# Kernel tuning notes

Measured on AMD Instinct MI355X. Metric: run time of the kernel, lower is better.

The kernel has to match this reference:

```python
import jax, jax.numpy as jnp
import numpy as np

B, T, C = 8, 2048, 1024
NEG_INF = -1e38


def setup_inputs() -> dict:
    key = jax.random.key(0)
    ks = jax.random.split(key, 10)
    s = 1.0 / np.sqrt(C)
    return {
        "x": jax.random.normal(ks[0], (B, T, C), jnp.float32),
        "Wk": jax.random.normal(ks[1], (C, C), jnp.float32) * s,
        "Wv": jax.random.normal(ks[2], (C, C), jnp.float32) * s,
        "Wr": jax.random.normal(ks[3], (C, C), jnp.float32) * s,
        "Wo": jax.random.normal(ks[4], (C, C), jnp.float32) * s,
        "time_decay": jax.random.normal(ks[5], (C,), jnp.float32) * 0.5,
        "time_first": jax.random.normal(ks[6], (C,), jnp.float32) * 0.5,
        "time_mix_key": jax.random.uniform(ks[7], (1, 1, C), jnp.float32),
        "time_mix_value": jax.random.uniform(ks[8], (1, 1, C), jnp.float32),
        "time_mix_receptance": jax.random.uniform(ks[9], (1, 1, C), jnp.float32),
    }


def _wkv(k, v, time_decay, time_first):
    # k, v: [B, T, C]; numerically-stabilized exp-sum recurrence over T
    w = -jnp.exp(time_decay)  # [C]
    u = time_first            # [C]

    def step(carry, kv):
        num, den, mx = carry
        kt, vt = kv  # [B, C]
        # output at this step uses u bonus
        m_out = jnp.maximum(mx, kt + u)
        e1 = jnp.exp(mx - m_out)
        e2 = jnp.exp(kt + u - m_out)
        out = (e1 * num + e2 * vt) / (e1 * den + e2)
        # state update with decay w
        m_new = jnp.maximum(mx + w, kt)
        e1 = jnp.exp(mx + w - m_new)
        e2 = jnp.exp(kt - m_new)
        return (e1 * num + e2 * vt, e1 * den + e2, m_new), out

    init = (jnp.zeros((B, C), jnp.float32),
            jnp.zeros((B, C), jnp.float32),
            jnp.full((B, C), NEG_INF, jnp.float32))
    kT = jnp.swapaxes(k, 0, 1)  # [T, B, C]
    vT = jnp.swapaxes(v, 0, 1)
    _, outs = jax.lax.scan(step, init, (kT, vT))
    return jnp.swapaxes(outs, 0, 1)  # [B, T, C]


def reference(x, Wk, Wv, Wr, Wo, time_decay, time_first,
              time_mix_key, time_mix_value, time_mix_receptance):
    # time_shift: prev_x[t] = x[t-1], zero at t=0
    prev_x = jnp.concatenate([jnp.zeros_like(x[:, :1]), x[:, :-1]], axis=1)

    r_in = x * time_mix_receptance + prev_x * (1 - time_mix_receptance)
    k_in = x * time_mix_key + prev_x * (1 - time_mix_key)
    v_in = x * time_mix_value + prev_x * (1 - time_mix_value)

    receptance = jnp.einsum('btc,dc->btd', r_in, Wr)
    key = jnp.einsum('btc,dc->btd', k_in, Wk)
    value = jnp.einsum('btc,dc->btd', v_in, Wv)

    wkv = _wkv(key, value, time_decay, time_first)
    rwkv = jax.nn.sigmoid(receptance) * wkv
    return jnp.einsum('btc,dc->btd', rwkv, Wo)
```

## Files before the change

### kernel.cpp

```cpp
#include <hip/hip_runtime.h>
#include <cstdint>
#include <cstddef>

#define DEVI __device__ __forceinline__

typedef __attribute__((ext_vector_type(8))) short short8;
typedef __attribute__((ext_vector_type(4))) float f32x4;

constexpr int Bc = 8, Tc = 2048, Cc = 1024;
constexpr int WKV_L = 32, WKV_NCH = 64;

DEVI unsigned short f2b(float f) {
  unsigned int u = __float_as_uint(f);
  unsigned int r = (u + 0x7FFFu + ((u >> 16) & 1u)) >> 16;
  return (unsigned short)r;
}
DEVI float b2f(unsigned short u) {
  return __uint_as_float(((unsigned int)u) << 16);
}

DEVI void gload16(const unsigned short* g, unsigned short* l) {
  __builtin_amdgcn_global_load_lds(
      (const __attribute__((address_space(1))) void*)g,
      (__attribute__((address_space(3))) void*)l, 16, 0, 0);
}

__global__ void convert_bf16_kernel(const float* __restrict__ in,
                                    unsigned short* __restrict__ out, int n4) {
  int i = blockIdx.x * blockDim.x + threadIdx.x;
  if (i >= n4) return;
  const float4 v = ((const float4*)in)[i];
  ushort4 o;
  o.x = f2b(v.x); o.y = f2b(v.y); o.z = f2b(v.z); o.w = f2b(v.w);
  ((ushort4*)out)[i] = o;
}

__global__ void mix3_kernel(const float* __restrict__ x,
                            const float* __restrict__ tmk,
                            const float* __restrict__ tmv,
                            const float* __restrict__ tmr,
                            unsigned short* __restrict__ kin,
                            unsigned short* __restrict__ vin,
                            unsigned short* __restrict__ rin,
                            long n4) {
  long i = (long)blockIdx.x * blockDim.x + threadIdx.x;
  const long stride = (long)gridDim.x * blockDim.x;
  for (; i < n4; i += stride) {
    const long e = i * 4;
    const int c = (int)(e & (Cc - 1));
    const long bt = e >> 10;
    const int t = (int)(bt & (Tc - 1));
    const float4 xv = *(const float4*)(x + e);
    float4 pv = {0.f, 0.f, 0.f, 0.f};
    if (t > 0) pv = *(const float4*)(x + e - Cc);
    const float4 mk = *(const float4*)(tmk + c);
    const float4 mv = *(const float4*)(tmv + c);
    const float4 mr = *(const float4*)(tmr + c);
    const float* xp = (const float*)&xv;
    const float* pp = (const float*)&pv;
    const float* mkp = (const float*)&mk;
    const float* mvp = (const float*)&mv;
    const float* mrp = (const float*)&mr;
    ushort4 ko, vo, ro;
    unsigned short* kop = (unsigned short*)&ko;
    unsigned short* vop = (unsigned short*)&vo;
    unsigned short* rop = (unsigned short*)&ro;
#pragma unroll
    for (int q = 0; q < 4; ++q) {
      kop[q] = f2b(xp[q] * mkp[q] + pp[q] * (1.f - mkp[q]));
      vop[q] = f2b(xp[q] * mvp[q] + pp[q] * (1.f - mvp[q]));
      rop[q] = f2b(xp[q] * mrp[q] + pp[q] * (1.f - mrp[q]));
    }
    *(ushort4*)(kin + e) = ko;
    *(ushort4*)(vin + e) = vo;
    *(ushort4*)(rin + e) = ro;
  }
}

template <typename OutT>
__global__ __launch_bounds__(512, 2)
void gemm256(const unsigned short* __restrict__ A0,
             const unsigned short* __restrict__ W0, OutT* __restrict__ C0,
             const unsigned short* __restrict__ A1,
             const unsigned short* __restrict__ W1, OutT* __restrict__ C1,
             const unsigned short* __restrict__ A2,
             const unsigned short* __restrict__ W2, OutT* __restrict__ C2,
             int K, int N) {
  constexpr int BK = 64;
  __shared__ alignas(16) unsigned short As[2][256 * BK];
  __shared__ alignas(16) unsigned short Bs[2][256 * BK];
  const int z = blockIdx.z;
  const unsigned short* A = z == 0 ? A0 : (z == 1 ? A1 : A2);
  const unsigned short* W = z == 0 ? W0 : (z == 1 ? W1 : W2);
  OutT* C_out = z == 0 ? C0 : (z == 1 ? C1 : C2);
  const int m0 = blockIdx.x * 256;
  const int n0 = blockIdx.y * 256;
  const int tid = threadIdx.x;
  const int lane = tid & 63;
  const int w = tid >> 6;
  const int wm = w >> 2;
  const int wn = w & 3;
  const int fr = lane & 15;
  const int ksl = lane >> 4;

  f32x4 acc[8][4];
#pragma unroll
  for (int i = 0; i < 8; ++i)
#pragma unroll
    for (int j = 0; j < 4; ++j) acc[i][j] = (f32x4){0.f, 0.f, 0.f, 0.f};

#define STAGE(buf, kt)                                                        \
  {                                                                           \
    _Pragma("unroll")                                                         \
    for (int cc = 0; cc < 4; ++cc) {                                          \
      const int c = w * 256 + cc * 64 + lane;                                 \
      const int row = c >> 3;                                                 \
      const int gsl = (c & 7) ^ (row & 7);                                    \
      gload16(A + (size_t)(m0 + row) * K + (kt) + gsl * 8,                    \
              &As[buf][(w * 256 + cc * 64) * 8]);                             \
      gload16(W + (size_t)(n0 + row) * K + (kt) + gsl * 8,                    \
              &Bs[buf][(w * 256 + cc * 64) * 8]);                             \
    }                                                                         \
  }

  const int nt = K / BK;
  STAGE(0, 0);
  int cur = 0;
  for (int t = 0; t < nt; ++t) {
    asm volatile("s_waitcnt vmcnt(0)" ::: "memory");
    __builtin_amdgcn_s_barrier();
    asm volatile("" ::: "memory");
    if (t + 1 < nt) STAGE(cur ^ 1, (t + 1) * BK);
#pragma unroll
    for (int ks = 0; ks < 2; ++ks) {
      const int sl = ks * 4 + ksl;
      short8 af[8], bf[4];
#pragma unroll
      for (int i = 0; i < 8; ++i) {
        const int row = wm * 128 + i * 16 + fr;
        af[i] = *(const short8*)&As[cur][row * 64 + ((sl ^ (row & 7)) * 8)];
      }
#pragma unroll
      for (int j = 0; j < 4; ++j) {
        const int row = wn * 64 + j * 16 + fr;
        bf[j] = *(const short8*)&Bs[cur][row * 64 + ((sl ^ (row & 7)) * 8)];
      }
      __builtin_amdgcn_s_setprio(1);
#pragma unroll
      for (int i = 0; i < 8; ++i)
#pragma unroll
        for (int j = 0; j < 4; ++j)
          acc[i][j] = __builtin_amdgcn_mfma_f32_16x16x32_bf16(af[i], bf[j],
                                                              acc[i][j], 0, 0, 0);
      __builtin_amdgcn_s_setprio(0);
    }
    asm volatile("" ::: "memory");
    cur ^= 1;
  }
#undef STAGE

  const int orow = (lane >> 4) * 4;
  const int ocol = lane & 15;
#pragma unroll
  for (int i = 0; i < 8; ++i)
#pragma unroll
    for (int j = 0; j < 4; ++j) {
      const size_t rbase = (size_t)(m0 + wm * 128 + i * 16 + orow);
      const int cb = n0 + wn * 64 + j * 16 + ocol;
#pragma unroll
      for (int q = 0; q < 4; ++q) {
        const float vq = acc[i][j][q];
        if constexpr (sizeof(OutT) == 2)
          C_out[(rbase + q) * N + cb] = (OutT)f2b(vq);
        else
          C_out[(rbase + q) * N + cb] = (OutT)vq;
      }
    }
}

__global__ void wkv_phase1(const unsigned short* __restrict__ keyb,
                           const unsigned short* __restrict__ valb,
                           const float* __restrict__ td,
                           float* __restrict__ s_num,
                           float* __restrict__ s_den,
                           float* __restrict__ s_mx) {
  const int g = blockIdx.x * blockDim.x + threadIdx.x;
  const int c = g & (Cc - 1);
  const int j = (g / Cc) & (WKV_NCH - 1);
  const int b = g / (Cc * WKV_NCH);
  const float w = -__expf(td[c]);
  float num = 0.f, den = 0.f, mx = -1e38f;
  size_t idx = ((size_t)b * Tc + (size_t)j * WKV_L) * Cc + c;
#pragma unroll 4
  for (int i = 0; i < WKV_L; ++i, idx += Cc) {
    const float kt = b2f(keyb[idx]);
    const float vt = b2f(valb[idx]);
    const float mw = mx + w;
    const float mn = fmaxf(mw, kt);
    const float a1 = __expf(mw - mn);
    const float a2 = __expf(kt - mn);
    num = a1 * num + a2 * vt;
    den = a1 * den + a2;
    mx = mn;
  }
  s_num[g] = num; s_den[g] = den; s_mx[g] = mx;
}

__global__ void wkv_phase2(const float* __restrict__ td,
                           float* __restrict__ s_num,
                           float* __restrict__ s_den,
                           float* __restrict__ s_mx) {
  const int g = blockIdx.x * blockDim.x + threadIdx.x;
  const int c = g & (Cc - 1);
  const int b = g / Cc;
  const float Lw = -__expf(td[c]) * (float)WKV_L;
  float num = 0.f, den = 0.f, mx = -1e38f;
  size_t base = (size_t)b * WKV_NCH * Cc + c;
  for (int j = 0; j < WKV_NCH; ++j) {
    const size_t s = base + (size_t)j * Cc;
    const float ln = s_num[s], ld = s_den[s], lm = s_mx[s];
    s_num[s] = num; s_den[s] = den; s_mx[s] = mx;
    const float md = mx + Lw;
    const float m = fmaxf(md, lm);
    const float e1 = __expf(md - m);
    const float e2 = __expf(lm - m);
    num = e1 * num + e2 * ln;
    den = e1 * den + e2 * ld;
    mx = m;
  }
}

__global__ void wkv_phase3(const unsigned short* __restrict__ keyb,
                           const unsigned short* __restrict__ valb,
                           const unsigned short* __restrict__ recb,
                           const float* __restrict__ td,
                           const float* __restrict__ tf,
                           const float* __restrict__ s_num,
                           const float* __restrict__ s_den,
                           const float* __restrict__ s_mx,
                           unsigned short* __restrict__ rwkv) {
  const int g = blockIdx.x * blockDim.x + threadIdx.x;
  const int c = g & (Cc - 1);
  const int j = (g / Cc) & (WKV_NCH - 1);
  const int b = g / (Cc * WKV_NCH);
  const float w = -__expf(td[c]);
  const float u = tf[c];
  float num = s_num[g], den = s_den[g], mx = s_mx[g];
  size_t idx = ((size_t)b * Tc + (size_t)j * WKV_L) * Cc + c;
#pragma unroll 2
  for (int i = 0; i < WKV_L; ++i, idx += Cc) {
    const float kt = b2f(keyb[idx]);
    const float vt = b2f(valb[idx]);
    const float rt = b2f(recb[idx]);
    const float ku = kt + u;
    const float mo = fmaxf(mx, ku);
    const float e1 = __expf(mx - mo);
    const float e2 = __expf(ku - mo);
    const float out = (e1 * num + e2 * vt) / (e1 * den + e2);
    const float sr = 1.f / (1.f + __expf(-rt));
    rwkv[idx] = f2b(sr * out);
    const float mw = mx + w;
    const float mn = fmaxf(mw, kt);
    const float a1 = __expf(mw - mn);
    const float a2 = __expf(kt - mn);
    num = a1 * num + a2 * vt;
    den = a1 * den + a2;
    mx = mn;
  }
}

extern "C" void kernel_launch(void* const* d_in, const int* in_sizes, int n_in,
                              void* d_out, int out_size, void* d_ws, size_t ws_size,
                              hipStream_t stream) {
  const float* x   = (const float*)d_in[0];
  const float* Wk  = (const float*)d_in[1];
  const float* Wv  = (const float*)d_in[2];
  const float* Wr  = (const float*)d_in[3];
  const float* Wo  = (const float*)d_in[4];
  const float* td  = (const float*)d_in[5];
  const float* tf  = (const float*)d_in[6];
  const float* tmk = (const float*)d_in[7];
  const float* tmv = (const float*)d_in[8];
  const float* tmr = (const float*)d_in[9];

  const long BT = (long)Bc * Tc;
  const long NE = BT * Cc;
  const long CC = (long)Cc * Cc;

  char* p = (char*)d_ws;
  unsigned short* Wk_b = (unsigned short*)p; p += CC * 2;
  unsigned short* Wv_b = (unsigned short*)p; p += CC * 2;
  unsigned short* Wr_b = (unsigned short*)p; p += CC * 2;
  unsigned short* Wo_b = (unsigned short*)p; p += CC * 2;
  unsigned short* kin  = (unsigned short*)p; p += NE * 2;
  unsigned short* vin  = (unsigned short*)p; p += NE * 2;
  unsigned short* rin  = (unsigned short*)p; p += NE * 2;
  unsigned short* keyb = (unsigned short*)p; p += NE * 2;
  unsigned short* valb = (unsigned short*)p; p += NE * 2;
  unsigned short* recb = (unsigned short*)p; p += NE * 2;
  unsigned short* rwkv = kin;
  const long NS = (long)Bc * WKV_NCH * Cc;
  float* s_num = (float*)vin;
  float* s_den = s_num + NS;
  float* s_mx  = s_den + NS;

  {
    const int n4 = (int)(CC / 4);
    dim3 g((n4 + 255) / 256), b_(256);
    convert_bf16_kernel<<<g, b_, 0, stream>>>(Wk, Wk_b, n4);
    convert_bf16_kernel<<<g, b_, 0, stream>>>(Wv, Wv_b, n4);
    convert_bf16_kernel<<<g, b_, 0, stream>>>(Wr, Wr_b, n4);
    convert_bf16_kernel<<<g, b_, 0, stream>>>(Wo, Wo_b, n4);
  }

  mix3_kernel<<<2048, 256, 0, stream>>>(x, tmk, tmv, tmr, kin, vin, rin, NE / 4);

  {
    dim3 grid((unsigned)(BT / 256), (unsigned)(Cc / 256), 3), blk(512);
    gemm256<unsigned short><<<grid, blk, 0, stream>>>(
        kin, Wk_b, keyb, vin, Wv_b, valb, rin, Wr_b, recb, Cc, Cc);
  }

  wkv_phase1<<<2048, 256, 0, stream>>>(keyb, valb, td, s_num, s_den, s_mx);
  wkv_phase2<<<32, 256, 0, stream>>>(td, s_num, s_den, s_mx);
  wkv_phase3<<<2048, 256, 0, stream>>>(keyb, valb, recb, td, tf,
                                       s_num, s_den, s_mx, rwkv);

  {
    dim3 grid((unsigned)(BT / 256), (unsigned)(Cc / 256), 1), blk(512);
    gemm256<float><<<grid, blk, 0, stream>>>(
        rwkv, Wo_b, (float*)d_out, rwkv, Wo_b, (float*)d_out,
        rwkv, Wo_b, (float*)d_out, Cc, Cc);
  }
}
```

Baseline: 266.9 us.

## Interleave LDS fragment loads with MFMAs, merge weight converts, single-exp WKV updates

The GEMM inner loop is restructured so LDS reads for the next group of fragments are issued between MFMA groups, with the k-slice split into halves. The intent is to hide LDS latency behind matrix math. It also drops the s_setprio calls. The four weight-conversion launches are merged into one 2D-grid launch to cut launch overhead. The WKV recurrences now compute a single exp per max-stabilised step by branching on which operand is larger, halving transcendental work at the cost of selects.

```diff
diff --git a/kernel.cpp b/kernel.cpp
--- a/kernel.cpp
+++ b/kernel.cpp
@@ -25,10 +25,20 @@
       (__attribute__((address_space(3))) void*)l, 16, 0, 0);
 }
 
-__global__ void convert_bf16_kernel(const float* __restrict__ in,
-                                    unsigned short* __restrict__ out, int n4) {
-  int i = blockIdx.x * blockDim.x + threadIdx.x;
-  if (i >= n4) return;
+#define FENCE() asm volatile("" ::: "memory")
+
+__global__ void convert4_kernel(const float* __restrict__ W0,
+                                const float* __restrict__ W1,
+                                const float* __restrict__ W2,
+                                const float* __restrict__ W3,
+                                unsigned short* __restrict__ o0,
+                                unsigned short* __restrict__ o1,
+                                unsigned short* __restrict__ o2,
+                                unsigned short* __restrict__ o3) {
+  const int i = blockIdx.x * blockDim.x + threadIdx.x;
+  const int s = blockIdx.y;
+  const float* in = s == 0 ? W0 : (s == 1 ? W1 : (s == 2 ? W2 : W3));
+  unsigned short* out = s == 0 ? o0 : (s == 1 ? o1 : (s == 2 ? o2 : o3));
   const float4 v = ((const float4*)in)[i];
   ushort4 o;
   o.x = f2b(v.x); o.y = f2b(v.y); o.z = f2b(v.z); o.w = f2b(v.w);
@@ -123,41 +133,69 @@
     }                                                                         \
   }
 
+#define LDSRD(bufp, row, sl) \
+  (*(const short8*)&(bufp)[(row) * 64 + ((((sl) ^ ((row) & 7))) * 8)])
+
   const int nt = K / BK;
   STAGE(0, 0);
   int cur = 0;
   for (int t = 0; t < nt; ++t) {
     asm volatile("s_waitcnt vmcnt(0)" ::: "memory");
     __builtin_amdgcn_s_barrier();
-    asm volatile("" ::: "memory");
+    FENCE();
     if (t + 1 < nt) STAGE(cur ^ 1, (t + 1) * BK);
-#pragma unroll
-    for (int ks = 0; ks < 2; ++ks) {
-      const int sl = ks * 4 + ksl;
-      short8 af[8], bf[4];
-#pragma unroll
-      for (int i = 0; i < 8; ++i) {
-        const int row = wm * 128 + i * 16 + fr;
-        af[i] = *(const short8*)&As[cur][row * 64 + ((sl ^ (row & 7)) * 8)];
-      }
-#pragma unroll
-      for (int j = 0; j < 4; ++j) {
-        const int row = wn * 64 + j * 16 + fr;
-        bf[j] = *(const short8*)&Bs[cur][row * 64 + ((sl ^ (row & 7)) * 8)];
-      }
-      __builtin_amdgcn_s_setprio(1);
-#pragma unroll
-      for (int i = 0; i < 8; ++i)
-#pragma unroll
-        for (int j = 0; j < 4; ++j)
-          acc[i][j] = __builtin_amdgcn_mfma_f32_16x16x32_bf16(af[i], bf[j],
-                                                              acc[i][j], 0, 0, 0);
-      __builtin_amdgcn_s_setprio(0);
-    }
-    asm volatile("" ::: "memory");
+    const unsigned short* Ab = As[cur];
+    const unsigned short* Bb = Bs[cur];
+    const int sl0 = ksl;
+    const int sl1 = 4 + ksl;
+    short8 a0[4], b0[4], a1g[4], a2g[4], b2[4], a3[4];
+#pragma unroll
+    for (int i = 0; i < 4; ++i)
+      a0[i] = LDSRD(Ab, wm * 128 + i * 16 + fr, sl0);
+#pragma unroll
+    for (int j = 0; j < 4; ++j)
+      b0[j] = LDSRD(Bb, wn * 64 + j * 16 + fr, sl0);
+#pragma unroll
+    for (int i = 0; i < 4; ++i)
+      a1g[i] = LDSRD(Ab, wm * 128 + (4 + i) * 16 + fr, sl0);
+#pragma unroll
+    for (int i = 0; i < 4; ++i)
+#pragma unroll
+      for (int j = 0; j < 4; ++j)
+        acc[i][j] = __builtin_amdgcn_mfma_f32_16x16x32_bf16(a0[i], b0[j],
+                                                            acc[i][j], 0, 0, 0);
+#pragma unroll
+    for (int i = 0; i < 4; ++i)
+      a2g[i] = LDSRD(Ab, wm * 128 + i * 16 + fr, sl1);
+#pragma unroll
+    for (int j = 0; j < 4; ++j)
+      b2[j] = LDSRD(Bb, wn * 64 + j * 16 + fr, sl1);
+#pragma unroll
+    for (int i = 0; i < 4; ++i)
+#pragma unroll
+      for (int j = 0; j < 4; ++j)
+        acc[4 + i][j] = __builtin_amdgcn_mfma_f32_16x16x32_bf16(a1g[i], b0[j],
+                                                                acc[4 + i][j], 0, 0, 0);
+#pragma unroll
+    for (int i = 0; i < 4; ++i)
+      a3[i] = LDSRD(Ab, wm * 128 + (4 + i) * 16 + fr, sl1);
+#pragma unroll
+    for (int i = 0; i < 4; ++i)
+#pragma unroll
+      for (int j = 0; j < 4; ++j)
+        acc[i][j] = __builtin_amdgcn_mfma_f32_16x16x32_bf16(a2g[i], b2[j],
+                                                            acc[i][j], 0, 0, 0);
+#pragma unroll
+    for (int i = 0; i < 4; ++i)
+#pragma unroll
+      for (int j = 0; j < 4; ++j)
+        acc[4 + i][j] = __builtin_amdgcn_mfma_f32_16x16x32_bf16(a3[i], b2[j],
+                                                                acc[4 + i][j], 0, 0, 0);
+    FENCE();
     cur ^= 1;
   }
 #undef STAGE
+#undef LDSRD
 
   const int orow = (lane >> 4) * 4;
   const int ocol = lane & 15;
@@ -196,12 +234,13 @@
     const float kt = b2f(keyb[idx]);
     const float vt = b2f(valb[idx]);
     const float mw = mx + w;
-    const float mn = fmaxf(mw, kt);
-    const float a1 = __expf(mw - mn);
-    const float a2 = __expf(kt - mn);
+    const bool cg = mw >= kt;
+    const float d = __expf(cg ? kt - mw : mw - kt);
+    const float a1 = cg ? 1.f : d;
+    const float a2 = cg ? d : 1.f;
     num = a1 * num + a2 * vt;
     den = a1 * den + a2;
-    mx = mn;
+    mx = cg ? mw : kt;
   }
   s_num[g] = num; s_den[g] = den; s_mx[g] = mx;
 }
@@ -221,12 +260,13 @@
     const float ln = s_num[s], ld = s_den[s], lm = s_mx[s];
     s_num[s] = num; s_den[s] = den; s_mx[s] = mx;
     const float md = mx + Lw;
-    const float m = fmaxf(md, lm);
-    const float e1 = __expf(md - m);
-    const float e2 = __expf(lm - m);
+    const bool cg = md >= lm;
+    const float d = __expf(cg ? lm - md : md - lm);
+    const float e1 = cg ? 1.f : d;
+    const float e2 = cg ? d : 1.f;
     num = e1 * num + e2 * ln;
     den = e1 * den + e2 * ld;
-    mx = m;
+    mx = cg ? md : lm;
   }
 }
 
@@ -253,19 +293,21 @@
     const float vt = b2f(valb[idx]);
     const float rt = b2f(recb[idx]);
     const float ku = kt + u;
-    const float mo = fmaxf(mx, ku);
-    const float e1 = __expf(mx - mo);
-    const float e2 = __expf(ku - mo);
+    const bool co = mx >= ku;
+    const float dd = __expf(co ? ku - mx : mx - ku);
+    const float e1 = co ? 1.f : dd;
+    const float e2 = co ? dd : 1.f;
     const float out = (e1 * num + e2 * vt) / (e1 * den + e2);
     const float sr = 1.f / (1.f + __expf(-rt));
     rwkv[idx] = f2b(sr * out);
     const float mw = mx + w;
-    const float mn = fmaxf(mw, kt);
-    const float a1 = __expf(mw - mn);
-    const float a2 = __expf(kt - mn);
+    const bool cg = mw >= kt;
+    const float du = __expf(cg ? kt - mw : mw - kt);
+    const float a1 = cg ? 1.f : du;
+    const float a2 = cg ? du : 1.f;
     num = a1 * num + a2 * vt;
     den = a1 * den + a2;
-    mx = mn;
+    mx = cg ? mw : kt;
   }
 }
 
@@ -305,12 +347,9 @@
   float* s_mx  = s_den + NS;
 
   {
-    const int n4 = (int)(CC / 4);
-    dim3 g((n4 + 255) / 256), b_(256);
-    convert_bf16_kernel<<<g, b_, 0, stream>>>(Wk, Wk_b, n4);
-    convert_bf16_kernel<<<g, b_, 0, stream>>>(Wv, Wv_b, n4);
-    convert_bf16_kernel<<<g, b_, 0, stream>>>(Wr, Wr_b, n4);
-    convert_bf16_kernel<<<g, b_, 0, stream>>>(Wo, Wo_b, n4);
+    dim3 g((unsigned)(CC / 4 / 256), 4), b_(256);
+    convert4_kernel<<<g, b_, 0, stream>>>(Wk, Wv, Wr, Wo,
+                                          Wk_b, Wv_b, Wr_b, Wo_b);
   }
 
   mix3_kernel<<<2048, 256, 0, stream>>>(x, tmk, tmv, tmr, kin, vin, rin, NE / 4);
```

Result: no change. 267.8 us (+0.3%).
